# Kernel optimization log

Hardware: AMD Instinct MI355X
Metric: run time of the kernel (lower is better)

The kernel has to match this reference:

```python
import jax, jax.numpy as jnp
import numpy as np

D_MODEL = 1024
NUM_HEADS = 16
B, S = 1, 4096


def setup_inputs() -> dict:
    key = jax.random.key(0)
    kx, kq, kk, kv, ko = jax.random.split(key, 5)
    std = (1.0 / D_MODEL) ** 0.5
    def trunc(k):
        return std * jax.random.truncated_normal(k, -3.0, 3.0, (D_MODEL, D_MODEL), dtype=jnp.float32)
    return {
        "x": jax.random.normal(kx, (B, S, D_MODEL), dtype=jnp.float32),
        "W_Q": trunc(kq),
        "W_K": trunc(kk),
        "W_V": trunc(kv),
        "W_O": trunc(ko),
    }


def reference(x, W_Q, W_K, W_V, W_O):
    Bx, Sx, Dm = x.shape
    H = NUM_HEADS
    d_attn = Dm // H
    # projections (torch code uses x @ W.T)
    Q = x @ W_Q.T
    K = x @ W_K.T
    V = x @ W_V.T
    # [B, H, S, d]
    Q = Q.reshape(Bx, Sx, H, d_attn).transpose(0, 2, 1, 3)
    K = K.reshape(Bx, Sx, H, d_attn).transpose(0, 2, 1, 3)
    V = V.reshape(Bx, Sx, H, d_attn).transpose(0, 2, 1, 3)
    scale = 1.0 / jnp.sqrt(jnp.asarray(d_attn, dtype=x.dtype))
    # [B, H, S, S] scores
    attn = jnp.einsum("bhqd,bhkd->bhqk", Q, K) * scale
    causal = jnp.tril(jnp.ones((Sx, Sx), dtype=bool))
    attn = jnp.where(causal, attn, jnp.asarray(-jnp.inf, dtype=attn.dtype))
    probs = jax.nn.softmax(attn, axis=-1)
    y = jnp.einsum("bhqk,bhkd->bhqd", probs, V)
    y = y.transpose(0, 2, 1, 3).reshape(Bx, Sx, Dm)
    return y @ W_O.T
```

## Files before the change

### kernel.cpp

```cpp
#include <hip/hip_runtime.h>

#define S_LEN 4096
#define DMODEL 1024
#define NHEADS 16

typedef __attribute__((ext_vector_type(8))) short bf16x8;
typedef __attribute__((ext_vector_type(4))) float f32x4;
typedef unsigned short u16;
typedef unsigned int u32;
typedef unsigned long long u64;

#define MEMFENCE asm volatile("" ::: "memory")

__device__ inline u16 f2bf(float f) {
    union { float f; u32 u; } v; v.f = f;
    u32 r = v.u + 0x7fffu + ((v.u >> 16) & 1u);
    return (u16)(r >> 16);
}

__device__ inline u32 pkbf2(float a, float b) {
    union { float f; u32 u; } ua, ub; ua.f = a; ub.f = b;
    const u32 ra = ua.u + 0x7fffu + ((ua.u >> 16) & 1u);
    const u32 rb = ub.u + 0x7fffu + ((ub.u >> 16) & 1u);
    return __builtin_amdgcn_perm(rb, ra, 0x07060302u);
}

__device__ inline u32 pkbf2f(float a, float b) {
    union { float f; u32 u; } ua, ub; ua.f = a; ub.f = b;
    const u32 ra = ua.u + 0x8000u;
    const u32 rb = ub.u + 0x8000u;
    return __builtin_amdgcn_perm(rb, ra, 0x07060302u);
}

__device__ inline void cp16(const void* g, void* l) {
    __builtin_amdgcn_global_load_lds(
        (const __attribute__((address_space(1))) unsigned int*)g,
        (__attribute__((address_space(3))) unsigned int*)l, 16, 0, 0);
}

__global__ __launch_bounds__(256) void cvt_all(const float* __restrict__ x,
                                               const float* __restrict__ wq,
                                               const float* __restrict__ wk,
                                               const float* __restrict__ wv,
                                               const float* __restrict__ wo,
                                               u16* __restrict__ xb,
                                               u16* __restrict__ w3,
                                               u16* __restrict__ wob) {
    const int b = blockIdx.x;
    const float* s; u16* d; int off;
    const int NW = DMODEL * DMODEL;
    if (b < 2048)      { s = x;  d = xb;          off = b * 2048; }
    else if (b < 2560) { s = wq; d = w3;          off = (b - 2048) * 2048; }
    else if (b < 3072) { s = wk; d = w3 + NW;     off = (b - 2560) * 2048; }
    else if (b < 3584) { s = wv; d = w3 + 2 * NW; off = (b - 3072) * 2048; }
    else               { s = wo; d = wob;         off = (b - 3584) * 2048; }
    const int i = off + threadIdx.x * 8;
    const float4 a = *(const float4*)(s + i);
    const float4 c = *(const float4*)(s + i + 4);
    u16 t[8];
    t[0] = f2bf(a.x); t[1] = f2bf(a.y); t[2] = f2bf(a.z); t[3] = f2bf(a.w);
    t[4] = f2bf(c.x); t[5] = f2bf(c.y); t[6] = f2bf(c.z); t[7] = f2bf(c.w);
    *(bf16x8*)(d + i) = *(const bf16x8*)t;
}

__global__ __launch_bounds__(256) void gemm_qkv(const u16* __restrict__ A,
                                                const u16* __restrict__ B3,
                                                u16* __restrict__ Qo,
                                                u16* __restrict__ Ko,
                                                u16* __restrict__ Vo) {
    __shared__ __align__(16) u16 As[2][128 * 32];
    __shared__ __align__(16) u16 Bs[2][128 * 32];
    const int tid = threadIdx.x, lane = tid & 63, wave = tid >> 6;
    const int wm = (wave >> 1) * 64, wn = (wave & 1) * 64;
    const int m0 = blockIdx.y * 128, n0 = blockIdx.x * 128;
    const int l15 = lane & 15, quad = lane >> 4;
    const bool swapAB = (n0 < 2048);

    f32x4 acc[4][4];
#pragma unroll
    for (int i = 0; i < 4; i++)
#pragma unroll
        for (int j = 0; j < 4; j++) acc[i][j] = (f32x4){0.f, 0.f, 0.f, 0.f};

    const int r0 = tid >> 2, c0 = (tid & 3) * 8;

    cp16(A + (size_t)(m0 + r0) * 1024 + c0,       As[0] + r0 * 32 + c0);
    cp16(A + (size_t)(m0 + r0 + 64) * 1024 + c0,  As[0] + (r0 + 64) * 32 + c0);
    cp16(B3 + (size_t)(n0 + r0) * 1024 + c0,      Bs[0] + r0 * 32 + c0);
    cp16(B3 + (size_t)(n0 + r0 + 64) * 1024 + c0, Bs[0] + (r0 + 64) * 32 + c0);

    int cur = 0;
    for (int kk = 0; kk < 1024; kk += 32) {
        __syncthreads();
        if (kk + 32 < 1024) {
            const int kn = kk + 32;
            cp16(A + (size_t)(m0 + r0) * 1024 + kn + c0,       As[cur ^ 1] + r0 * 32 + c0);
            cp16(A + (size_t)(m0 + r0 + 64) * 1024 + kn + c0,  As[cur ^ 1] + (r0 + 64) * 32 + c0);
            cp16(B3 + (size_t)(n0 + r0) * 1024 + kn + c0,      Bs[cur ^ 1] + r0 * 32 + c0);
            cp16(B3 + (size_t)(n0 + r0 + 64) * 1024 + kn + c0, Bs[cur ^ 1] + (r0 + 64) * 32 + c0);
        }
        bf16x8 af[4], bfr[4];
#pragma unroll
        for (int i = 0; i < 4; i++)
            af[i] = *(const bf16x8*)(As[cur] + (wm + i * 16 + l15) * 32 + quad * 8);
#pragma unroll
        for (int j = 0; j < 4; j++)
            bfr[j] = *(const bf16x8*)(Bs[cur] + (wn + j * 16 + l15) * 32 + quad * 8);
        if (swapAB) {
#pragma unroll
            for (int i = 0; i < 4; i++)
#pragma unroll
                for (int j = 0; j < 4; j++)
                    acc[i][j] = __builtin_amdgcn_mfma_f32_16x16x32_bf16(bfr[j], af[i], acc[i][j], 0, 0, 0);
        } else {
#pragma unroll
            for (int i = 0; i < 4; i++)
#pragma unroll
                for (int j = 0; j < 4; j++)
                    acc[i][j] = __builtin_amdgcn_mfma_f32_16x16x32_bf16(af[i], bfr[j], acc[i][j], 0, 0, 0);
        }
        cur ^= 1;
    }

    const int which = n0 >> 10;
    const int n0r = n0 & 1023;
    u16* dst = (which == 0) ? Qo : (which == 1) ? Ko : Vo;
    const int h = (n0r + wn) >> 6;
    u16* base = dst + (size_t)h * S_LEN * 64;
    if (which < 2) {
        const float sc = (which == 0) ? 0.125f * 1.4426950408889634f : 1.0f;
#pragma unroll
        for (int i = 0; i < 4; i++) {
            const int row = m0 + wm + i * 16 + l15;
#pragma unroll
            for (int j = 0; j < 4; j++) {
                const int c = j * 16 + quad * 4;
                const u32 y0 = pkbf2(acc[i][j][0] * sc, acc[i][j][1] * sc);
                const u32 y1 = pkbf2(acc[i][j][2] * sc, acc[i][j][3] * sc);
                *(u64*)(base + (size_t)row * 64 + c) = (u64)y0 | ((u64)y1 << 32);
            }
        }
    } else {
#pragma unroll
        for (int i = 0; i < 4; i++) {
            const int row0 = m0 + wm + i * 16 + quad * 4;
#pragma unroll
            for (int j = 0; j < 4; j++) {
                const int c = j * 16 + l15;
                const u32 y0 = pkbf2(acc[i][j][0], acc[i][j][1]);
                const u32 y1 = pkbf2(acc[i][j][2], acc[i][j][3]);
                *(u64*)(base + (size_t)c * S_LEN + row0) = (u64)y0 | ((u64)y1 << 32);
            }
        }
    }
}

__global__ __launch_bounds__(256) void gemm_out(const u16* __restrict__ A,
                                                const u16* __restrict__ B,
                                                float* __restrict__ C) {
    __shared__ __align__(16) u16 As[2][64 * 64];
    __shared__ __align__(16) u16 Bs[2][128 * 64];
    const int tid = threadIdx.x, lane = tid & 63, wave = tid >> 6;
    const int wm = (wave >> 1) * 32, wn = (wave & 1) * 64;
    const int bx = blockIdx.x;
    const int n0 = (bx & 7) * 128, m0 = (bx >> 3) * 64;
    const int l15 = lane & 15, quad = lane >> 4;
    const int swz = l15 & 7;

    f32x4 acc[2][4];
#pragma unroll
    for (int i = 0; i < 2; i++)
#pragma unroll
        for (int j = 0; j < 4; j++) acc[i][j] = (f32x4){0.f, 0.f, 0.f, 0.f};

#define STAGE_OUT(buf, kb)                                                              \
    {                                                                                   \
        _Pragma("unroll")                                                               \
        for (int q = 0; q < 2; q++) {                                                   \
            const int ch = tid + q * 256;                                               \
            const int ar = ch >> 3, ac = ((ch & 7) ^ (ar & 7)) * 8;                     \
            cp16(A + (size_t)(m0 + ar) * 1024 + (kb) + ac, As[buf] + ch * 8);           \
        }                                                                               \
        _Pragma("unroll")                                                               \
        for (int q = 0; q < 4; q++) {                                                   \
            const int ch = tid + q * 256;                                               \
            const int br = ch >> 3, bc = ((ch & 7) ^ (br & 7)) * 8;                     \
            cp16(B + (size_t)(n0 + br) * 1024 + (kb) + bc, Bs[buf] + ch * 8);           \
        }                                                                               \
    }

    STAGE_OUT(0, 0);
    int cur = 0;
    for (int kk = 0; kk < 1024; kk += 64) {
        __syncthreads();
        if (kk + 64 < 1024) STAGE_OUT(cur ^ 1, kk + 64);
#pragma unroll
        for (int h = 0; h < 2; h++) {
            const int cc = (h * 4 + quad) ^ swz;
            bf16x8 af[2], bfr[4];
#pragma unroll
            for (int i = 0; i < 2; i++)
                af[i] = *(const bf16x8*)(As[cur] + (wm + i * 16 + l15) * 64 + cc * 8);
#pragma unroll
            for (int j = 0; j < 4; j++)
                bfr[j] = *(const bf16x8*)(Bs[cur] + (wn + j * 16 + l15) * 64 + cc * 8);
#pragma unroll
            for (int i = 0; i < 2; i++)
#pragma unroll
                for (int j = 0; j < 4; j++)
                    acc[i][j] = __builtin_amdgcn_mfma_f32_16x16x32_bf16(bfr[j], af[i], acc[i][j], 0, 0, 0);
        }
        cur ^= 1;
    }
#undef STAGE_OUT

#pragma unroll
    for (int i = 0; i < 2; i++) {
        const int row = m0 + wm + i * 16 + l15;
#pragma unroll
        for (int j = 0; j < 4; j++) {
            const int col = n0 + wn + j * 16 + quad * 4;
            *(f32x4*)(C + (size_t)row * 1024 + col) = acc[i][j];
        }
    }
}

__global__ __launch_bounds__(256, 3) void attn(const u16* __restrict__ Q,
                                               const u16* __restrict__ Kh,
                                               const u16* __restrict__ Vt,
                                               u16* __restrict__ Y) {
    __shared__ __align__(16) u16 KW[2][4][2048];
    __shared__ __align__(16) u16 VW[4][2048];
    const int b = blockIdx.x;
    const int head = b & 15;
    const int jq = 63 - (b >> 4);
    const int nkt = jq + 1;
    const int np = (nkt + 1) >> 1;
    const int qa = jq * 64;
    const int tid = threadIdx.x, lane = tid & 63, w = tid >> 6;
    const int l15 = lane & 15, quad = lane >> 4;
    const int swz = l15 & 7;

    const u16* Qp = Q + (size_t)head * S_LEN * 64;
    const u16* Kp = Kh + (size_t)head * S_LEN * 64;
    const u16* Vp = Vt + (size_t)head * 64 * S_LEN;

    bf16x8 qf[4][2];
#pragma unroll
    for (int qg = 0; qg < 4; qg++)
#pragma unroll
        for (int h = 0; h < 2; h++)
            qf[qg][h] = *(const bf16x8*)(Qp + (size_t)(qa + qg * 16 + l15) * 64 + h * 32 + quad * 8);
    MEMFENCE;

    f32x4 o[4][4];
#pragma unroll
    for (int dg = 0; dg < 4; dg++)
#pragma unroll
        for (int qg = 0; qg < 4; qg++) o[dg][qg] = (f32x4){0.f, 0.f, 0.f, 0.f};
    float lp[4] = {0.f, 0.f, 0.f, 0.f};

    const int keyl = w * 16 + quad * 4;
    const int s4 = (l15 >> 1) & 3;
    const int ceo = (((quad >> 1) ^ s4)) * 8 + (quad & 1) * 4;
    const int coo = ceo ^ 16;

    union PU { u32 d[4]; bf16x8 v; };
    union VU { u64 d[2]; bf16x8 v; };

#define STAGE_K(buf, kp2)                                                               \
    {                                                                                   \
        _Pragma("unroll")                                                               \
        for (int i = 0; i < 4; i++) {                                                   \
            const int gk = (kp2) * 128 + w * 16 + (i & 1) * 8 + (lane >> 3) + (i >> 1) * 64; \
            const int lc = (lane & 7) ^ (lane >> 3);                                    \
            cp16(Kp + (size_t)gk * 64 + lc * 8, KW[buf][w] + i * 512 + lane * 8);       \
        }                                                                               \
    }

#define STAGE_V(kp2)                                                                    \
    {                                                                                   \
        _Pragma("unroll")                                                               \
        for (int i = 0; i < 4; i++) {                                                   \
            const int d = i * 16 + (lane >> 2);                                         \
            const int L = (lane & 3) ^ ((lane >> 3) & 3);                               \
            const int s = (kp2) * 128 + w * 16 + (L >> 1) * 64 + (L & 1) * 8;           \
            cp16(Vp + (size_t)d * S_LEN + s, VW[w] + i * 512 + lane * 8);               \
        }                                                                               \
    }

#define QK_PHASE(DGE, DGO, HO)                                                          \
    {                                                                                   \
        const u16* Kb = KW[cur][w];                                                     \
        const bf16x8 kE0 = *(const bf16x8*)(Kb + l15 * 64 + (quad ^ swz) * 8);          \
        const bf16x8 kE1 = *(const bf16x8*)(Kb + l15 * 64 + ((4 ^ quad) ^ swz) * 8);    \
        const bf16x8 kO0 = *(const bf16x8*)(Kb + (16 + l15) * 64 + (quad ^ swz) * 8);   \
        const bf16x8 kO1 = *(const bf16x8*)(Kb + (16 + l15) * 64 + ((4 ^ quad) ^ swz) * 8); \
        _Pragma("unroll")                                                               \
        for (int qg = 0; qg < 4; qg++) {                                                \
            const int ql = qg * 16 + l15;                                               \
            f32x4 c = (f32x4){0.f, 0.f, 0.f, 0.f};                                      \
            c = __builtin_amdgcn_mfma_f32_16x16x32_bf16(kE0, qf[qg][0], c, 0, 0, 0);    \
            c = __builtin_amdgcn_mfma_f32_16x16x32_bf16(kE1, qf[qg][1], c, 0, 0, 0);    \
            float p0 = __builtin_amdgcn_exp2f(c[0]);                                    \
            float p1 = __builtin_amdgcn_exp2f(c[1]);                                    \
            float p2 = __builtin_amdgcn_exp2f(c[2]);                                    \
            float p3 = __builtin_amdgcn_exp2f(c[3]);                                    \
            if (DGE) {                                                                  \
                if (keyl + 0 > ql) p0 = 0.f;                                            \
                if (keyl + 1 > ql) p1 = 0.f;                                            \
                if (keyl + 2 > ql) p2 = 0.f;                                            \
                if (keyl + 3 > ql) p3 = 0.f;                                            \
            }                                                                           \
            lp[qg] += (p0 + p1) + (p2 + p3);                                            \
            pu[qg].d[0] = pkbf2f(p0, p1);                                               \
            pu[qg].d[1] = pkbf2f(p2, p3);                                               \
            if (HO) {                                                                   \
                f32x4 cc = (f32x4){0.f, 0.f, 0.f, 0.f};                                 \
                cc = __builtin_amdgcn_mfma_f32_16x16x32_bf16(kO0, qf[qg][0], cc, 0, 0, 0); \
                cc = __builtin_amdgcn_mfma_f32_16x16x32_bf16(kO1, qf[qg][1], cc, 0, 0, 0); \
                float q0 = __builtin_amdgcn_exp2f(cc[0]);                               \
                float q1 = __builtin_amdgcn_exp2f(cc[1]);                               \
                float q2 = __builtin_amdgcn_exp2f(cc[2]);                               \
                float q3 = __builtin_amdgcn_exp2f(cc[3]);                               \
                if (DGO) {                                                              \
                    if (keyl + 0 > ql) q0 = 0.f;                                        \
                    if (keyl + 1 > ql) q1 = 0.f;                                        \
                    if (keyl + 2 > ql) q2 = 0.f;                                        \
                    if (keyl + 3 > ql) q3 = 0.f;                                        \
                }                                                                       \
                lp[qg] += (q0 + q1) + (q2 + q3);                                        \
                pu[qg].d[2] = pkbf2f(q0, q1);                                           \
                pu[qg].d[3] = pkbf2f(q2, q3);                                           \
            } else {                                                                    \
                pu[qg].d[2] = 0u; pu[qg].d[3] = 0u;                                     \
            }                                                                           \
        }                                                                               \
    }

#define PV_PHASE()                                                                      \
    {                                                                                   \
        _Pragma("unroll")                                                               \
        for (int dg = 0; dg < 4; dg++) {                                                \
            const u16* vb = VW[w] + (dg * 16 + l15) * 32;                               \
            VU vf;                                                                      \
            vf.d[0] = *(const u64*)(vb + ceo);                                          \
            vf.d[1] = *(const u64*)(vb + coo);                                          \
            _Pragma("unroll")                                                           \
            for (int qg = 0; qg < 4; qg++)                                              \
                o[dg][qg] = __builtin_amdgcn_mfma_f32_16x16x32_bf16(vf.v, pu[qg].v, o[dg][qg], 0, 0, 0); \
        }                                                                               \
    }

    STAGE_K(0, 0);
    MEMFENCE;
    STAGE_V(0);
    MEMFENCE;

    int cur = 0;
    for (int kp = 0; kp < np - 1; kp++) {
        STAGE_K(cur ^ 1, kp + 1);
        asm volatile("s_waitcnt vmcnt(8)" ::: "memory");
        __builtin_amdgcn_sched_barrier(0);
        PU pu[4];
        QK_PHASE(false, false, true);
        asm volatile("s_waitcnt vmcnt(4)" ::: "memory");
        __builtin_amdgcn_sched_barrier(0);
        PV_PHASE();
        MEMFENCE;
        STAGE_V(kp + 1);
        MEMFENCE;
        cur ^= 1;
    }
    {
        asm volatile("s_waitcnt vmcnt(4)" ::: "memory");
        __builtin_amdgcn_sched_barrier(0);
        const bool dE = !(jq & 1);
        const bool hO = (jq & 1);
        PU pu[4];
        QK_PHASE(dE, true, hO);
        asm volatile("s_waitcnt vmcnt(0)" ::: "memory");
        __builtin_amdgcn_sched_barrier(0);
        PV_PHASE();
    }
#undef STAGE_K
#undef STAGE_V
#undef QK_PHASE
#undef PV_PHASE

    float* OR = (float*)&KW[0][0][0];
    float* LR = (float*)((char*)&KW[0][0][0] + 24576);
#pragma unroll
    for (int qg = 0; qg < 4; qg++) {
        lp[qg] += __shfl_xor(lp[qg], 16);
        lp[qg] += __shfl_xor(lp[qg], 32);
    }
    __syncthreads();
    if (lane < 16) {
#pragma unroll
        for (int qg = 0; qg < 4; qg++) LR[(w * 4 + qg) * 16 + lane] = lp[qg];
    }
    const int qrow = tid >> 2;
    const int qgr = qrow >> 4, lq = qrow & 15;
    const int dpart = (tid & 3) * 4;
    __syncthreads();
    const float lsum = LR[qgr * 16 + lq] + LR[(4 + qgr) * 16 + lq] +
                       LR[(8 + qgr) * 16 + lq] + LR[(12 + qgr) * 16 + lq];
    const float inv = 1.f / lsum;
#pragma unroll
    for (int dg = 0; dg < 4; dg++) {
        if (dg) __syncthreads();
#pragma unroll
        for (int qg = 0; qg < 4; qg++)
            *(f32x4*)&OR[((w * 4 + qg) * 16 + l15) * 20 + quad * 4] = o[dg][qg];
        __syncthreads();
        f32x4 s = (f32x4){0.f, 0.f, 0.f, 0.f};
#pragma unroll
        for (int sw = 0; sw < 4; sw++)
            s += *(const f32x4*)&OR[((sw * 4 + qgr) * 16 + lq) * 20 + dpart];
        const u32 y0 = pkbf2(s[0] * inv, s[1] * inv);
        const u32 y1 = pkbf2(s[2] * inv, s[3] * inv);
        *(u64*)(Y + (size_t)(qa + qrow) * DMODEL + head * 64 + dg * 16 + dpart) =
            (u64)y0 | ((u64)y1 << 32);
    }
}

extern "C" void kernel_launch(void* const* d_in, const int* in_sizes, int n_in,
                              void* d_out, int out_size, void* d_ws, size_t ws_size,
                              hipStream_t stream) {
    const float* x  = (const float*)d_in[0];
    const float* wq = (const float*)d_in[1];
    const float* wk = (const float*)d_in[2];
    const float* wv = (const float*)d_in[3];
    const float* wo = (const float*)d_in[4];
    float* out = (float*)d_out;

    u16* qh  = (u16*)d_ws;
    u16* kh  = qh + (size_t)S_LEN * DMODEL;
    u16* vt  = kh + (size_t)S_LEN * DMODEL;
    u16* xb  = vt + (size_t)S_LEN * DMODEL;
    u16* y   = xb;
    u16* wb3 = xb + (size_t)S_LEN * DMODEL;
    u16* wob = wb3 + (size_t)3 * DMODEL * DMODEL;

    const dim3 blk(256);

    cvt_all<<<4096, blk, 0, stream>>>(x, wq, wk, wv, wo, xb, wb3, wob);
    gemm_qkv<<<dim3(3 * DMODEL / 128, S_LEN / 128), blk, 0, stream>>>(xb, wb3, qh, kh, vt);
    attn<<<1024, blk, 0, stream>>>(qh, kh, vt, y);
    gemm_out<<<512, blk, 0, stream>>>(y, wob, out);
}
```

Before: 208.6 us.

## Triple-buffer QKV GEMM LDS tiles with explicit vmcnt-gated prefetch

Replaces the double-buffered K loop of the QKV projection GEMM with a three-stage LDS ring. Two tiles are prefetched ahead, and a partial s_waitcnt vmcnt(4) lets the newest loads stay in flight across the barrier. The goal is to hide global-to-LDS latency better than the previous full wait per step. The cost is 50% more shared memory per block, which may lower occupancy. Correctness also depends on cp16's async semantics matching the vmcnt counting.

```diff
diff --git a/kernel.cpp b/kernel.cpp
--- a/kernel.cpp
+++ b/kernel.cpp
@@ -68,8 +68,8 @@
                                                 u16* __restrict__ Qo,
                                                 u16* __restrict__ Ko,
                                                 u16* __restrict__ Vo) {
-    __shared__ __align__(16) u16 As[2][128 * 32];
-    __shared__ __align__(16) u16 Bs[2][128 * 32];
+    __shared__ __align__(16) u16 As[3][128 * 32];
+    __shared__ __align__(16) u16 Bs[3][128 * 32];
     const int tid = threadIdx.x, lane = tid & 63, wave = tid >> 6;
     const int wm = (wave >> 1) * 64, wn = (wave & 1) * 64;
     const int m0 = blockIdx.y * 128, n0 = blockIdx.x * 128;
@@ -84,43 +84,59 @@
 
     const int r0 = tid >> 2, c0 = (tid & 3) * 8;
 
-    cp16(A + (size_t)(m0 + r0) * 1024 + c0,       As[0] + r0 * 32 + c0);
-    cp16(A + (size_t)(m0 + r0 + 64) * 1024 + c0,  As[0] + (r0 + 64) * 32 + c0);
-    cp16(B3 + (size_t)(n0 + r0) * 1024 + c0,      Bs[0] + r0 * 32 + c0);
-    cp16(B3 + (size_t)(n0 + r0 + 64) * 1024 + c0, Bs[0] + (r0 + 64) * 32 + c0);
-
-    int cur = 0;
-    for (int kk = 0; kk < 1024; kk += 32) {
-        __syncthreads();
-        if (kk + 32 < 1024) {
-            const int kn = kk + 32;
-            cp16(A + (size_t)(m0 + r0) * 1024 + kn + c0,       As[cur ^ 1] + r0 * 32 + c0);
-            cp16(A + (size_t)(m0 + r0 + 64) * 1024 + kn + c0,  As[cur ^ 1] + (r0 + 64) * 32 + c0);
-            cp16(B3 + (size_t)(n0 + r0) * 1024 + kn + c0,      Bs[cur ^ 1] + r0 * 32 + c0);
-            cp16(B3 + (size_t)(n0 + r0 + 64) * 1024 + kn + c0, Bs[cur ^ 1] + (r0 + 64) * 32 + c0);
+#define STAGE_QKV(buf, kkb)                                                        \
+    {                                                                              \
+        cp16(A + (size_t)(m0 + r0) * 1024 + (kkb) + c0,       As[buf] + r0 * 32 + c0); \
+        cp16(A + (size_t)(m0 + r0 + 64) * 1024 + (kkb) + c0,  As[buf] + (r0 + 64) * 32 + c0); \
+        cp16(B3 + (size_t)(n0 + r0) * 1024 + (kkb) + c0,      Bs[buf] + r0 * 32 + c0); \
+        cp16(B3 + (size_t)(n0 + r0 + 64) * 1024 + (kkb) + c0, Bs[buf] + (r0 + 64) * 32 + c0); \
+    }
+
+#define COMPUTE_QKV(cur)                                                           \
+    {                                                                              \
+        bf16x8 af[4], bfr[4];                                                      \
+        _Pragma("unroll")                                                          \
+        for (int i = 0; i < 4; i++)                                                \
+            af[i] = *(const bf16x8*)(As[cur] + (wm + i * 16 + l15) * 32 + quad * 8); \
+        _Pragma("unroll")                                                          \
+        for (int j = 0; j < 4; j++)                                                \
+            bfr[j] = *(const bf16x8*)(Bs[cur] + (wn + j * 16 + l15) * 32 + quad * 8); \
+        if (swapAB) {                                                              \
+            _Pragma("unroll")                                                      \
+            for (int i = 0; i < 4; i++)                                            \
+                _Pragma("unroll")                                                  \
+                for (int j = 0; j < 4; j++)                                        \
+                    acc[i][j] = __builtin_amdgcn_mfma_f32_16x16x32_bf16(bfr[j], af[i], acc[i][j], 0, 0, 0); \
+        } else {                                                                   \
+            _Pragma("unroll")                                                      \
+            for (int i = 0; i < 4; i++)                                            \
+                _Pragma("unroll")                                                  \
+                for (int j = 0; j < 4; j++)                                        \
+                    acc[i][j] = __builtin_amdgcn_mfma_f32_16x16x32_bf16(af[i], bfr[j], acc[i][j], 0, 0, 0); \
+        }                                                                          \
+    }
+
+    STAGE_QKV(0, 0);
+    MEMFENCE;
+    STAGE_QKV(1, 32);
+    MEMFENCE;
+
+    for (int ks = 0; ks < 31; ks++) {
+        asm volatile("s_waitcnt vmcnt(4)" ::: "memory");
+        __builtin_amdgcn_s_barrier();
+        __builtin_amdgcn_sched_barrier(0);
+        if (ks < 30) {
+            STAGE_QKV((ks + 2) % 3, (ks + 2) * 32);
+            MEMFENCE;
         }
-        bf16x8 af[4], bfr[4];
-#pragma unroll
-        for (int i = 0; i < 4; i++)
-            af[i] = *(const bf16x8*)(As[cur] + (wm + i * 16 + l15) * 32 + quad * 8);
-#pragma unroll
-        for (int j = 0; j < 4; j++)
-            bfr[j] = *(const bf16x8*)(Bs[cur] + (wn + j * 16 + l15) * 32 + quad * 8);
-        if (swapAB) {
-#pragma unroll
-            for (int i = 0; i < 4; i++)
-#pragma unroll
-                for (int j = 0; j < 4; j++)
-                    acc[i][j] = __builtin_amdgcn_mfma_f32_16x16x32_bf16(bfr[j], af[i], acc[i][j], 0, 0, 0);
-        } else {
-#pragma unroll
-            for (int i = 0; i < 4; i++)
-#pragma unroll
-                for (int j = 0; j < 4; j++)
-                    acc[i][j] = __builtin_amdgcn_mfma_f32_16x16x32_bf16(af[i], bfr[j], acc[i][j], 0, 0, 0);
-        }
-        cur ^= 1;
-    }
+        COMPUTE_QKV(ks % 3);
+    }
+    asm volatile("s_waitcnt vmcnt(0)" ::: "memory");
+    __builtin_amdgcn_s_barrier();
+    __builtin_amdgcn_sched_barrier(0);
+    COMPUTE_QKV(1);
+#undef STAGE_QKV
+#undef COMPUTE_QKV
 
     const int which = n0 >> 10;
     const int n0r = n0 & 1023;
```

New measurement: 211.1 us. Within noise of the previous version (+1.2%).
